# Optimization experiments

Hardware: AMD Instinct MI355X
Metric: run time of the kernel (lower is better)

The kernel has to match this reference:

```python
import jax, jax.numpy as jnp
import numpy as np

NUM_NODES = 100000
OUT_CHANNELS = 64
NUM_EDGES = 3200000


def setup_inputs() -> dict:
    key = jax.random.key(0)
    k1, k2, k3 = jax.random.split(key, 3)
    edge_index = jax.random.randint(k1, (2, NUM_EDGES), 0, NUM_NODES, dtype=jnp.int64) if jax.config.jax_enable_x64 else jax.random.randint(k1, (2, NUM_EDGES), 0, NUM_NODES, dtype=jnp.int32)
    # nn.Linear default init: U(-1/sqrt(fan_in), 1/sqrt(fan_in)); use randn-scale for a correctness baseline
    W_weight = jax.random.normal(k2, (OUT_CHANNELS, NUM_NODES), dtype=jnp.float32) * (1.0 / np.sqrt(NUM_NODES))
    W_bias = jax.random.normal(k3, (OUT_CHANNELS,), dtype=jnp.float32) * (1.0 / np.sqrt(NUM_NODES))
    return {"edge_index": edge_index, "W_weight": W_weight, "W_bias": W_bias}


def reference(edge_index, W_weight, W_bias):
    # A is the [N, N] binary COO adjacency (duplicate edges sum, matching
    # an uncoalesced torch sparse COO matmul). logits = A @ W_weight.T + b.
    num_nodes = W_weight.shape[1]
    row = edge_index[0] - jnp.min(edge_index[0])  # row = row - row.min()
    col = edge_index[1]
    Wt = W_weight.T  # [N, C]
    # SpMM as gather + segment-sum: logits[i] = sum_{(i,j) in E} Wt[j]
    logits = jax.ops.segment_sum(Wt[col], row, num_segments=num_nodes)  # [N, C]
    logits = logits + W_bias
    return jax.nn.log_softmax(logits, axis=1)
```

## Files before the change

### kernel.cpp

```cpp
#include <hip/hip_runtime.h>
#include <hip/hip_bf16.h>
#include <limits.h>

#define NUM_NODES 100000
#define OUT_CH 64
#define NUM_EDGES 3200000
#define BROWS 64
#define BSHIFT 6
#define NBUCK 1563
#define NPBLK 256
#define EPB (NUM_EDGES / NPBLK)
#define I4PB (EPB / 4)
#define STAGECAP 4096
#define NTRANS 1563

__global__ __launch_bounds__(256) void LINK_62689342652831_mintrans_kernel(
    const float* __restrict__ W, unsigned short* __restrict__ Wtb,
    const int* __restrict__ rows, int* __restrict__ minp) {
    __shared__ float tile[64][65];
    if (blockIdx.x < NTRANS) {
        int n0 = blockIdx.x * 64;
        int tx = threadIdx.x & 63;
        int ty = threadIdx.x >> 6;
        for (int c = ty; c < 64; c += 4) {
            int n = n0 + tx;
            tile[c][tx] = (n < NUM_NODES) ? W[(size_t)c * NUM_NODES + n] : 0.0f;
        }
        __syncthreads();
        for (int i = ty; i < 64; i += 4) {
            int n = n0 + i;
            if (n < NUM_NODES) {
                __hip_bfloat16 bv = __float2bfloat16(tile[tx][i]);
                Wtb[(size_t)n * OUT_CH + tx] = *(unsigned short*)&bv;
            }
        }
    } else {
        int blk = blockIdx.x - NTRANS;
        int tid = blk * 256 + threadIdx.x;
        int stride = 256 * 256;
        const int4* r4 = (const int4*)rows;
        int m = INT_MAX;
        for (int i = tid; i < NUM_EDGES / 4; i += stride) {
            int4 v = r4[i];
            m = min(m, min(min(v.x, v.y), min(v.z, v.w)));
        }
        for (int off = 32; off > 0; off >>= 1) m = min(m, __shfl_xor(m, off, 64));
        int* sm = (int*)tile;
        if ((threadIdx.x & 63) == 0) sm[threadIdx.x >> 6] = m;
        __syncthreads();
        if (threadIdx.x == 0) {
            int mm = min(min(sm[0], sm[1]), min(sm[2], sm[3]));
            atomicMin(minp, mm);
        }
    }
}

__global__ __launch_bounds__(512) void LINK_62689342652831_hist2d_kernel(
    const int* __restrict__ rows, const int* __restrict__ minp,
    int* __restrict__ hist2d) {
    __shared__ int h[NBUCK];
    for (int i = threadIdx.x; i < NBUCK; i += 512) h[i] = 0;
    __syncthreads();
    int minv = *minp;
    int blk = blockIdx.x;
    const int4* r4 = (const int4*)rows;
    for (int i = threadIdx.x; i < I4PB; i += 512) {
        int4 v = r4[blk * I4PB + i];
        atomicAdd(&h[(unsigned)(v.x - minv) >> BSHIFT], 1);
        atomicAdd(&h[(unsigned)(v.y - minv) >> BSHIFT], 1);
        atomicAdd(&h[(unsigned)(v.z - minv) >> BSHIFT], 1);
        atomicAdd(&h[(unsigned)(v.w - minv) >> BSHIFT], 1);
    }
    __syncthreads();
    for (int i = threadIdx.x; i < NBUCK; i += 512) hist2d[blk * NBUCK + i] = h[i];
}

__global__ __launch_bounds__(512) void LINK_62689342652831_colscan_kernel(
    int* __restrict__ hist2d, int* __restrict__ totals) {
    int lane = threadIdx.x & 63;
    int wid = threadIdx.x >> 6;
    int b = blockIdx.x * 8 + wid;
    if (b >= NBUCK) return;
    int carry = 0;
    for (int rnd = 0; rnd < NPBLK / 64; ++rnd) {
        int blk = rnd * 64 + lane;
        int v = hist2d[blk * NBUCK + b];
        int x = v;
        for (int off = 1; off < 64; off <<= 1) {
            int y = __shfl_up(x, off, 64);
            if (lane >= off) x += y;
        }
        hist2d[blk * NBUCK + b] = x - v + carry;
        carry += __shfl(x, 63, 64);
    }
    if (lane == 0) totals[b] = carry;
}

__global__ __launch_bounds__(1024) void LINK_62689342652831_bscan_kernel(
    const int* __restrict__ totals, int* __restrict__ bstart) {
    __shared__ int ss[1024];
    int t = threadIdx.x;
    int i0 = 2 * t, i1 = 2 * t + 1;
    int v0 = (i0 < NBUCK) ? totals[i0] : 0;
    int v1 = (i1 < NBUCK) ? totals[i1] : 0;
    int p1 = v0 + v1;
    ss[t] = p1;
    __syncthreads();
    for (int off = 1; off < 1024; off <<= 1) {
        int x = (t >= off) ? ss[t - off] : 0;
        __syncthreads();
        ss[t] += x;
        __syncthreads();
    }
    int texcl = ss[t] - p1;
    if (i0 < NBUCK) bstart[i0] = texcl;
    if (i1 < NBUCK) bstart[i1] = texcl + v0;
    if (t == 1023) bstart[NBUCK] = ss[1023];
}

__global__ __launch_bounds__(512) void LINK_62689342652831_part_kernel(
    const int* __restrict__ rows, const int* __restrict__ cols,
    const int* __restrict__ minp, const int* __restrict__ hist2d,
    const int* __restrict__ bstart, unsigned int* __restrict__ packed) {
    __shared__ int offs_l[NBUCK];
    __shared__ int lcur[NBUCK];
    int blk = blockIdx.x;
    for (int i = threadIdx.x; i < NBUCK; i += 512) {
        offs_l[i] = bstart[i] + hist2d[blk * NBUCK + i];
        lcur[i] = 0;
    }
    __syncthreads();
    int minv = *minp;
    const int4* r4 = (const int4*)rows;
    const int4* c4 = (const int4*)cols;
    for (int i = threadIdx.x; i < I4PB; i += 512) {
        int4 rv = r4[blk * I4PB + i];
        int4 cv = c4[blk * I4PB + i];
#pragma unroll
        for (int k = 0; k < 4; ++k) {
            int r = ((k == 0) ? rv.x : (k == 1) ? rv.y : (k == 2) ? rv.z : rv.w) - minv;
            int c = (k == 0) ? cv.x : (k == 1) ? cv.y : (k == 2) ? cv.z : cv.w;
            int b = (unsigned)r >> BSHIFT;
            int pos = offs_l[b] + atomicAdd(&lcur[b], 1);
            packed[pos] = ((unsigned)(r & (BROWS - 1)) << 17) | (unsigned)c;
        }
    }
}

__global__ __launch_bounds__(256) void LINK_62689342652831_spmm_kernel(
    const unsigned int* __restrict__ packed, const int* __restrict__ bstart,
    const unsigned short* __restrict__ Wtb, const float* __restrict__ bias,
    float* __restrict__ out) {
    __shared__ unsigned int sorted[STAGECAP];
    __shared__ int rhist[BROWS];
    __shared__ int rstart[BROWS + 1];
    __shared__ int rcur[BROWS];

    int lane = threadIdx.x & 63;
    int wid = threadIdx.x >> 6;
    int b = blockIdx.x;
    int s = bstart[b], e = bstart[b + 1];
    int n = e - s;

    if (n <= STAGECAP) {
        if (threadIdx.x < BROWS) rhist[threadIdx.x] = 0;
        __syncthreads();
        for (int i = threadIdx.x; i < n; i += 256)
            atomicAdd(&rhist[packed[s + i] >> 17], 1);
        __syncthreads();
        if (threadIdx.x < 64) {
            int c0 = rhist[lane];
            int x0 = c0;
            for (int off = 1; off < 64; off <<= 1) {
                int y0 = __shfl_up(x0, off, 64);
                if (lane >= off) x0 += y0;
            }
            rstart[lane] = x0 - c0;
            rcur[lane] = x0 - c0;
            if (lane == 63) rstart[64] = x0;
        }
        __syncthreads();
        for (int i = threadIdx.x; i < n; i += 256) {
            unsigned int u = packed[s + i];
            int pos = atomicAdd(&rcur[u >> 17], 1);
            sorted[pos] = u;
        }
        __syncthreads();

        const uint2* Wt2 = (const uint2*)Wtb;
        int q = lane >> 4;
        int ql = lane & 15;
        float b0 = bias[4 * ql], b1 = bias[4 * ql + 1],
              b2 = bias[4 * ql + 2], b3 = bias[4 * ql + 3];

        for (int r = wid; r < BROWS; r += 4) {
            int gr = b * BROWS + r;
            if (gr >= NUM_NODES) continue;
            int s0 = rstart[r], e0 = rstart[r + 1];
            float a0 = 0, a1 = 0, a2 = 0, a3 = 0;
            int i = s0 + q;
            for (; i + 4 < e0; i += 8) {
                unsigned int ua = sorted[i], ub = sorted[i + 4];
                uint2 wa = Wt2[(size_t)(ua & 0x1FFFF) * 16 + ql];
                uint2 wb = Wt2[(size_t)(ub & 0x1FFFF) * 16 + ql];
                a0 += __uint_as_float(wa.x << 16);
                a1 += __uint_as_float(wa.x & 0xFFFF0000u);
                a2 += __uint_as_float(wa.y << 16);
                a3 += __uint_as_float(wa.y & 0xFFFF0000u);
                a0 += __uint_as_float(wb.x << 16);
                a1 += __uint_as_float(wb.x & 0xFFFF0000u);
                a2 += __uint_as_float(wb.y << 16);
                a3 += __uint_as_float(wb.y & 0xFFFF0000u);
            }
            for (; i < e0; i += 4) {
                unsigned int u = sorted[i];
                uint2 w = Wt2[(size_t)(u & 0x1FFFF) * 16 + ql];
                a0 += __uint_as_float(w.x << 16);
                a1 += __uint_as_float(w.x & 0xFFFF0000u);
                a2 += __uint_as_float(w.y << 16);
                a3 += __uint_as_float(w.y & 0xFFFF0000u);
            }
            a0 += __shfl_xor(a0, 32, 64); a1 += __shfl_xor(a1, 32, 64);
            a2 += __shfl_xor(a2, 32, 64); a3 += __shfl_xor(a3, 32, 64);
            a0 += __shfl_xor(a0, 16, 64); a1 += __shfl_xor(a1, 16, 64);
            a2 += __shfl_xor(a2, 16, 64); a3 += __shfl_xor(a3, 16, 64);

            float x0 = a0 + b0, x1 = a1 + b1, x2 = a2 + b2, x3 = a3 + b3;
            float m = fmaxf(fmaxf(x0, x1), fmaxf(x2, x3));
            for (int off = 8; off > 0; off >>= 1) m = fmaxf(m, __shfl_xor(m, off, 64));
            float ssum = expf(x0 - m) + expf(x1 - m) + expf(x2 - m) + expf(x3 - m);
            for (int off = 8; off > 0; off >>= 1) ssum += __shfl_xor(ssum, off, 64);
            float l = m + logf(ssum);
            if (lane < 16) {
                float4 o = {x0 - l, x1 - l, x2 - l, x3 - l};
                *(float4*)&out[(size_t)gr * OUT_CH + 4 * ql] = o;
            }
        }
    } else {
        float* acc = (float*)sorted;
        for (int i = threadIdx.x; i < BROWS * OUT_CH; i += 256) acc[i] = 0.0f;
        __syncthreads();
        for (int i = s + wid; i < e; i += 4) {
            unsigned int u = packed[i];
            float v = __uint_as_float((unsigned int)Wtb[(size_t)(u & 0x1FFFF) * OUT_CH + lane] << 16);
            atomicAdd(&acc[(u >> 17) * OUT_CH + lane], v);
        }
        __syncthreads();
        float bsv = bias[lane];
        for (int r = wid; r < BROWS; r += 4) {
            int gr = b * BROWS + r;
            if (gr >= NUM_NODES) continue;
            float x = acc[r * OUT_CH + lane] + bsv;
            float m = x;
            for (int off = 32; off > 0; off >>= 1) m = fmaxf(m, __shfl_xor(m, off, 64));
            float ex = expf(x - m);
            float ssum = ex;
            for (int off = 32; off > 0; off >>= 1) ssum += __shfl_xor(ssum, off, 64);
            out[(size_t)gr * OUT_CH + lane] = x - m - logf(ssum);
        }
    }
}

__global__ void LINK_62689342652831_minf_kernel(const int* __restrict__ rows, int n,
                                                int* __restrict__ minp) {
    int tid = blockIdx.x * blockDim.x + threadIdx.x;
    int stride = gridDim.x * blockDim.x;
    int m = INT_MAX;
    for (int i = tid; i < n; i += stride) m = min(m, rows[i]);
    for (int off = 32; off > 0; off >>= 1) m = min(m, __shfl_xor(m, off, 64));
    if ((threadIdx.x & 63) == 0) atomicMin(minp, m);
}

__global__ void LINK_62689342652831_scatter_kernel(const int* __restrict__ rows,
                                                   const int* __restrict__ cols,
                                                   const float* __restrict__ W,
                                                   const int* __restrict__ minp,
                                                   float* __restrict__ out) {
    int lane = threadIdx.x & 63;
    int gw = (blockIdx.x * blockDim.x + threadIdx.x) >> 6;
    int nw = (gridDim.x * blockDim.x) >> 6;
    int minv = *minp;
    for (int e = gw; e < NUM_EDGES; e += nw) {
        int r = rows[e] - minv;
        int c = cols[e];
        float v = W[(size_t)lane * NUM_NODES + c];
        unsafeAtomicAdd(&out[(size_t)r * 64 + lane], v);
    }
}

__global__ void LINK_62689342652831_logsoftmax_kernel(float* __restrict__ out,
                                                      const float* __restrict__ bias) {
    int lane = threadIdx.x & 63;
    int gw = (blockIdx.x * blockDim.x + threadIdx.x) >> 6;
    int nw = (gridDim.x * blockDim.x) >> 6;
    float b = bias[lane];
    for (int r = gw; r < NUM_NODES; r += nw) {
        float x = out[(size_t)r * 64 + lane] + b;
        float m = x;
        for (int off = 32; off > 0; off >>= 1) m = fmaxf(m, __shfl_xor(m, off, 64));
        float e = expf(x - m);
        float s = e;
        for (int off = 32; off > 0; off >>= 1) s += __shfl_xor(s, off, 64);
        out[(size_t)r * 64 + lane] = x - m - logf(s);
    }
}

extern "C" void kernel_launch(void* const* d_in, const int* in_sizes, int n_in,
                              void* d_out, int out_size, void* d_ws, size_t ws_size,
                              hipStream_t stream) {
    const int* edges = (const int*)d_in[0];
    const int* rows = edges;
    const int* cols = edges + NUM_EDGES;
    const float* W = (const float*)d_in[1];
    const float* bias = (const float*)d_in[2];
    float* out = (float*)d_out;

    char* ws = (char*)d_ws;
    const size_t OFF_MIN = 0;
    const size_t OFF_BSTART = 256;
    const size_t OFF_TOT = 8192;
    const size_t OFF_H2D = 16384;
    const size_t OFF_PACKED = 2 * 1024 * 1024;
    const size_t OFF_WTB = OFF_PACKED + (size_t)NUM_EDGES * 4;
    const size_t need = OFF_WTB + (size_t)NUM_NODES * OUT_CH * 2;

    int* minp = (int*)(ws + OFF_MIN);
    int* bstart = (int*)(ws + OFF_BSTART);
    int* totals = (int*)(ws + OFF_TOT);
    int* hist2d = (int*)(ws + OFF_H2D);
    unsigned int* packed = (unsigned int*)(ws + OFF_PACKED);
    unsigned short* Wtb = (unsigned short*)(ws + OFF_WTB);

    hipMemsetAsync(minp, 0x7f, sizeof(int), stream);

    if (ws_size >= need) {
        LINK_62689342652831_mintrans_kernel<<<NTRANS + 256, 256, 0, stream>>>(W, Wtb, rows, minp);
        LINK_62689342652831_hist2d_kernel<<<NPBLK, 512, 0, stream>>>(rows, minp, hist2d);
        LINK_62689342652831_colscan_kernel<<<(NBUCK + 7) / 8, 512, 0, stream>>>(hist2d, totals);
        LINK_62689342652831_bscan_kernel<<<1, 1024, 0, stream>>>(totals, bstart);
        LINK_62689342652831_part_kernel<<<NPBLK, 512, 0, stream>>>(rows, cols, minp, hist2d,
                                                                   bstart, packed);
        LINK_62689342652831_spmm_kernel<<<NBUCK, 256, 0, stream>>>(packed, bstart, Wtb,
                                                                   bias, out);
    } else {
        LINK_62689342652831_minf_kernel<<<2048, 256, 0, stream>>>(rows, NUM_EDGES, minp);
        hipMemsetAsync(d_out, 0, (size_t)out_size * sizeof(float), stream);
        LINK_62689342652831_scatter_kernel<<<2048, 256, 0, stream>>>(rows, cols, W, minp, out);
        LINK_62689342652831_logsoftmax_kernel<<<4096, 256, 0, stream>>>(out, bias);
    }
}
```

Before: 136.9 us.

## Bucket by raw row and use sub-bucket global cursors for partitioning

Builds the row histogram on raw row ids inside the transpose/min kernel instead of after the min is known, accumulating into a global sub-bucketed histogram with 16 sub-slots per bucket. This drops the separate histogram and column-scan kernels. The partition kernel now claims slots with global atomics on the sub-bucket cursors instead of shared per-block offsets. The min offset is applied only in the SpMM kernel, which launches extra blocks to cover shifted buckets. This cuts kernel launches and passes over the rows, at the cost of global atomic contention in partitioning and a larger single-block scan. Edge order within a bucket becomes nondeterministic, and raw row ids at or above 100032 would overflow the bucket arrays.

```diff
diff --git a/kernel.cpp b/kernel.cpp
--- a/kernel.cpp
+++ b/kernel.cpp
@@ -8,15 +8,18 @@
 #define BROWS 64
 #define BSHIFT 6
 #define NBUCK 1563
+#define NBUCK_EXT 3125
+#define NSUB 16
+#define NSS (NBUCK * NSUB)
 #define NPBLK 256
 #define EPB (NUM_EDGES / NPBLK)
 #define I4PB (EPB / 4)
 #define STAGECAP 4096
 #define NTRANS 1563
 
-__global__ __launch_bounds__(256) void LINK_62689342652831_mintrans_kernel(
+__global__ __launch_bounds__(256) void LINK_62689342652831_mth_kernel(
     const float* __restrict__ W, unsigned short* __restrict__ Wtb,
-    const int* __restrict__ rows, int* __restrict__ minp) {
+    const int* __restrict__ rows, int* __restrict__ minp, int* __restrict__ ghist) {
     __shared__ float tile[64][65];
     if (blockIdx.x < NTRANS) {
         int n0 = blockIdx.x * 64;
@@ -36,75 +39,46 @@
         }
     } else {
         int blk = blockIdx.x - NTRANS;
-        int tid = blk * 256 + threadIdx.x;
-        int stride = 256 * 256;
+        int sub = blk & (NSUB - 1);
+        int* h = (int*)tile;
+        int* sm = (int*)tile + 4096;
+        for (int i = threadIdx.x; i < NBUCK; i += 256) h[i] = 0;
+        __syncthreads();
         const int4* r4 = (const int4*)rows;
         int m = INT_MAX;
-        for (int i = tid; i < NUM_EDGES / 4; i += stride) {
-            int4 v = r4[i];
+        for (int i = threadIdx.x; i < I4PB; i += 256) {
+            int4 v = r4[blk * I4PB + i];
             m = min(m, min(min(v.x, v.y), min(v.z, v.w)));
+            atomicAdd(&h[(unsigned)v.x >> BSHIFT], 1);
+            atomicAdd(&h[(unsigned)v.y >> BSHIFT], 1);
+            atomicAdd(&h[(unsigned)v.z >> BSHIFT], 1);
+            atomicAdd(&h[(unsigned)v.w >> BSHIFT], 1);
         }
         for (int off = 32; off > 0; off >>= 1) m = min(m, __shfl_xor(m, off, 64));
-        int* sm = (int*)tile;
         if ((threadIdx.x & 63) == 0) sm[threadIdx.x >> 6] = m;
         __syncthreads();
-        if (threadIdx.x == 0) {
-            int mm = min(min(sm[0], sm[1]), min(sm[2], sm[3]));
-            atomicMin(minp, mm);
-        }
-    }
-}
-
-__global__ __launch_bounds__(512) void LINK_62689342652831_hist2d_kernel(
-    const int* __restrict__ rows, const int* __restrict__ minp,
-    int* __restrict__ hist2d) {
-    __shared__ int h[NBUCK];
-    for (int i = threadIdx.x; i < NBUCK; i += 512) h[i] = 0;
-    __syncthreads();
-    int minv = *minp;
-    int blk = blockIdx.x;
-    const int4* r4 = (const int4*)rows;
-    for (int i = threadIdx.x; i < I4PB; i += 512) {
-        int4 v = r4[blk * I4PB + i];
-        atomicAdd(&h[(unsigned)(v.x - minv) >> BSHIFT], 1);
-        atomicAdd(&h[(unsigned)(v.y - minv) >> BSHIFT], 1);
-        atomicAdd(&h[(unsigned)(v.z - minv) >> BSHIFT], 1);
-        atomicAdd(&h[(unsigned)(v.w - minv) >> BSHIFT], 1);
-    }
-    __syncthreads();
-    for (int i = threadIdx.x; i < NBUCK; i += 512) hist2d[blk * NBUCK + i] = h[i];
-}
-
-__global__ __launch_bounds__(512) void LINK_62689342652831_colscan_kernel(
-    int* __restrict__ hist2d, int* __restrict__ totals) {
-    int lane = threadIdx.x & 63;
-    int wid = threadIdx.x >> 6;
-    int b = blockIdx.x * 8 + wid;
-    if (b >= NBUCK) return;
-    int carry = 0;
-    for (int rnd = 0; rnd < NPBLK / 64; ++rnd) {
-        int blk = rnd * 64 + lane;
-        int v = hist2d[blk * NBUCK + b];
-        int x = v;
-        for (int off = 1; off < 64; off <<= 1) {
-            int y = __shfl_up(x, off, 64);
-            if (lane >= off) x += y;
-        }
-        hist2d[blk * NBUCK + b] = x - v + carry;
-        carry += __shfl(x, 63, 64);
-    }
-    if (lane == 0) totals[b] = carry;
+        for (int i = threadIdx.x; i < NBUCK; i += 256)
+            if (h[i]) atomicAdd(&ghist[i * NSUB + sub], h[i]);
+        if (threadIdx.x == 0)
+            atomicMin(minp, min(min(sm[0], sm[1]), min(sm[2], sm[3])));
+    }
 }
 
 __global__ __launch_bounds__(1024) void LINK_62689342652831_bscan_kernel(
-    const int* __restrict__ totals, int* __restrict__ bstart) {
+    const int* __restrict__ ghist, int* __restrict__ sstart, int* __restrict__ cursor) {
     __shared__ int ss[1024];
+    const int PT = 25;
     int t = threadIdx.x;
-    int i0 = 2 * t, i1 = 2 * t + 1;
-    int v0 = (i0 < NBUCK) ? totals[i0] : 0;
-    int v1 = (i1 < NBUCK) ? totals[i1] : 0;
-    int p1 = v0 + v1;
-    ss[t] = p1;
+    int base = t * PT;
+    int v[PT];
+    int run = 0;
+#pragma unroll
+    for (int k = 0; k < PT; ++k) {
+        int idx = base + k;
+        v[k] = (idx < NSS) ? ghist[idx] : 0;
+        run += v[k];
+    }
+    ss[t] = run;
     __syncthreads();
     for (int off = 1; off < 1024; off <<= 1) {
         int x = (t >= off) ? ss[t - off] : 0;
@@ -112,25 +86,21 @@
         ss[t] += x;
         __syncthreads();
     }
-    int texcl = ss[t] - p1;
-    if (i0 < NBUCK) bstart[i0] = texcl;
-    if (i1 < NBUCK) bstart[i1] = texcl + v0;
-    if (t == 1023) bstart[NBUCK] = ss[1023];
+    int acc = ss[t] - run;
+#pragma unroll
+    for (int k = 0; k < PT; ++k) {
+        int idx = base + k;
+        if (idx < NSS) { sstart[idx] = acc; cursor[idx] = acc; }
+        acc += v[k];
+    }
+    if (t == 1023) sstart[NSS] = acc;
 }
 
 __global__ __launch_bounds__(512) void LINK_62689342652831_part_kernel(
     const int* __restrict__ rows, const int* __restrict__ cols,
-    const int* __restrict__ minp, const int* __restrict__ hist2d,
-    const int* __restrict__ bstart, unsigned int* __restrict__ packed) {
-    __shared__ int offs_l[NBUCK];
-    __shared__ int lcur[NBUCK];
+    int* __restrict__ cursor, unsigned int* __restrict__ packed) {
     int blk = blockIdx.x;
-    for (int i = threadIdx.x; i < NBUCK; i += 512) {
-        offs_l[i] = bstart[i] + hist2d[blk * NBUCK + i];
-        lcur[i] = 0;
-    }
-    __syncthreads();
-    int minv = *minp;
+    int sub = blk & (NSUB - 1);
     const int4* r4 = (const int4*)rows;
     const int4* c4 = (const int4*)cols;
     for (int i = threadIdx.x; i < I4PB; i += 512) {
@@ -138,19 +108,19 @@
         int4 cv = c4[blk * I4PB + i];
 #pragma unroll
         for (int k = 0; k < 4; ++k) {
-            int r = ((k == 0) ? rv.x : (k == 1) ? rv.y : (k == 2) ? rv.z : rv.w) - minv;
+            int r = (k == 0) ? rv.x : (k == 1) ? rv.y : (k == 2) ? rv.z : rv.w;
             int c = (k == 0) ? cv.x : (k == 1) ? cv.y : (k == 2) ? cv.z : cv.w;
             int b = (unsigned)r >> BSHIFT;
-            int pos = offs_l[b] + atomicAdd(&lcur[b], 1);
+            int pos = atomicAdd(&cursor[b * NSUB + sub], 1);
             packed[pos] = ((unsigned)(r & (BROWS - 1)) << 17) | (unsigned)c;
         }
     }
 }
 
 __global__ __launch_bounds__(256) void LINK_62689342652831_spmm_kernel(
-    const unsigned int* __restrict__ packed, const int* __restrict__ bstart,
+    const unsigned int* __restrict__ packed, const int* __restrict__ sstart,
     const unsigned short* __restrict__ Wtb, const float* __restrict__ bias,
-    float* __restrict__ out) {
+    const int* __restrict__ minp, float* __restrict__ out) {
     __shared__ unsigned int sorted[STAGECAP];
     __shared__ int rhist[BROWS];
     __shared__ int rstart[BROWS + 1];
@@ -159,7 +129,10 @@
     int lane = threadIdx.x & 63;
     int wid = threadIdx.x >> 6;
     int b = blockIdx.x;
-    int s = bstart[b], e = bstart[b + 1];
+    int minv = *minp;
+    if (b * BROWS - minv >= NUM_NODES) return;
+    int s = 0, e = 0;
+    if (b < NBUCK) { s = sstart[b * NSUB]; e = sstart[(b + 1) * NSUB]; }
     int n = e - s;
 
     if (n <= STAGECAP) {
@@ -194,8 +167,8 @@
               b2 = bias[4 * ql + 2], b3 = bias[4 * ql + 3];
 
         for (int r = wid; r < BROWS; r += 4) {
-            int gr = b * BROWS + r;
-            if (gr >= NUM_NODES) continue;
+            int gr = b * BROWS + r - minv;
+            if (gr < 0 || gr >= NUM_NODES) continue;
             int s0 = rstart[r], e0 = rstart[r + 1];
             float a0 = 0, a1 = 0, a2 = 0, a3 = 0;
             int i = s0 + q;
@@ -248,8 +221,8 @@
         __syncthreads();
         float bsv = bias[lane];
         for (int r = wid; r < BROWS; r += 4) {
-            int gr = b * BROWS + r;
-            if (gr >= NUM_NODES) continue;
+            int gr = b * BROWS + r - minv;
+            if (gr < 0 || gr >= NUM_NODES) continue;
             float x = acc[r * OUT_CH + lane] + bsv;
             float m = x;
             for (int off = 32; off > 0; off >>= 1) m = fmaxf(m, __shfl_xor(m, off, 64));
@@ -317,31 +290,30 @@
 
     char* ws = (char*)d_ws;
     const size_t OFF_MIN = 0;
-    const size_t OFF_BSTART = 256;
-    const size_t OFF_TOT = 8192;
-    const size_t OFF_H2D = 16384;
-    const size_t OFF_PACKED = 2 * 1024 * 1024;
+    const size_t OFF_GHIST = 1024;
+    const size_t OFF_SSTART = 256 * 1024;
+    const size_t OFF_CUR = 512 * 1024;
+    const size_t OFF_PACKED = 1024 * 1024;
     const size_t OFF_WTB = OFF_PACKED + (size_t)NUM_EDGES * 4;
     const size_t need = OFF_WTB + (size_t)NUM_NODES * OUT_CH * 2;
 
     int* minp = (int*)(ws + OFF_MIN);
-    int* bstart = (int*)(ws + OFF_BSTART);
-    int* totals = (int*)(ws + OFF_TOT);
-    int* hist2d = (int*)(ws + OFF_H2D);
+    int* ghist = (int*)(ws + OFF_GHIST);
+    int* sstart = (int*)(ws + OFF_SSTART);
+    int* cursor = (int*)(ws + OFF_CUR);
     unsigned int* packed = (unsigned int*)(ws + OFF_PACKED);
     unsigned short* Wtb = (unsigned short*)(ws + OFF_WTB);
 
     hipMemsetAsync(minp, 0x7f, sizeof(int), stream);
 
     if (ws_size >= need) {
-        LINK_62689342652831_mintrans_kernel<<<NTRANS + 256, 256, 0, stream>>>(W, Wtb, rows, minp);
-        LINK_62689342652831_hist2d_kernel<<<NPBLK, 512, 0, stream>>>(rows, minp, hist2d);
-        LINK_62689342652831_colscan_kernel<<<(NBUCK + 7) / 8, 512, 0, stream>>>(hist2d, totals);
-        LINK_62689342652831_bscan_kernel<<<1, 1024, 0, stream>>>(totals, bstart);
-        LINK_62689342652831_part_kernel<<<NPBLK, 512, 0, stream>>>(rows, cols, minp, hist2d,
-                                                                   bstart, packed);
-        LINK_62689342652831_spmm_kernel<<<NBUCK, 256, 0, stream>>>(packed, bstart, Wtb,
-                                                                   bias, out);
+        hipMemsetAsync(ghist, 0, (size_t)NSS * sizeof(int), stream);
+        LINK_62689342652831_mth_kernel<<<NTRANS + NPBLK, 256, 0, stream>>>(W, Wtb, rows,
+                                                                           minp, ghist);
+        LINK_62689342652831_bscan_kernel<<<1, 1024, 0, stream>>>(ghist, sstart, cursor);
+        LINK_62689342652831_part_kernel<<<NPBLK, 512, 0, stream>>>(rows, cols, cursor, packed);
+        LINK_62689342652831_spmm_kernel<<<NBUCK_EXT, 256, 0, stream>>>(packed, sstart, Wtb,
+                                                                       bias, minp, out);
     } else {
         LINK_62689342652831_minf_kernel<<<2048, 256, 0, stream>>>(rows, NUM_EDGES, minp);
         hipMemsetAsync(d_out, 0, (size_t)out_size * sizeof(float), stream);
```

Measured after the change: 296.9 us. 2.17x slower.

## Store transposed weights in scaled FP8 and fuse row histogram into min/transpose pass

Applied to the files above, without the earlier changes.

Quantizes the transposed weight table to scaled FP8 E4M3 instead of bf16, which halves the bytes gathered per edge in the SpMM. It also merges the histogram pass into the min-reduction/transpose kernel by bucketing on raw row ids, and applies the row-min offset later in the SpMM, launching extra blocks to cover the shift. This removes one kernel launch and one full read of the rows array. The cost is a large loss of precision from FP8, which may break tolerance, plus some idle extra SpMM blocks.

```diff
diff --git a/kernel.cpp b/kernel.cpp
--- a/kernel.cpp
+++ b/kernel.cpp
@@ -1,5 +1,6 @@
 #include <hip/hip_runtime.h>
 #include <hip/hip_bf16.h>
+#include <hip/hip_fp8.h>
 #include <limits.h>
 
 #define NUM_NODES 100000
@@ -8,15 +9,26 @@
 #define BROWS 64
 #define BSHIFT 6
 #define NBUCK 1563
+#define NBUCK_EXT 3125
 #define NPBLK 256
 #define EPB (NUM_EDGES / NPBLK)
 #define I4PB (EPB / 4)
 #define STAGECAP 4096
 #define NTRANS 1563
-
-__global__ __launch_bounds__(256) void LINK_62689342652831_mintrans_kernel(
-    const float* __restrict__ W, unsigned short* __restrict__ Wtb,
-    const int* __restrict__ rows, int* __restrict__ minp) {
+#define FP8_SCALE 256.0f
+#define FP8_INV (1.0f / 256.0f)
+
+typedef float v2f __attribute__((ext_vector_type(2)));
+
+__device__ __forceinline__ float fp8_decode_slow(unsigned b) {
+    unsigned s = b >> 7, e = (b >> 3) & 0xF, m = b & 7;
+    float v = (e == 0) ? ldexpf((float)m, -9) : ldexpf((float)(8 + m), (int)e - 10);
+    return s ? -v : v;
+}
+
+__global__ __launch_bounds__(256) void LINK_62689342652831_mth_kernel(
+    const float* __restrict__ W, unsigned char* __restrict__ Wt8,
+    const int* __restrict__ rows, int* __restrict__ minp, int* __restrict__ hist2d) {
     __shared__ float tile[64][65];
     if (blockIdx.x < NTRANS) {
         int n0 = blockIdx.x * 64;
@@ -30,49 +42,33 @@
         for (int i = ty; i < 64; i += 4) {
             int n = n0 + i;
             if (n < NUM_NODES) {
-                __hip_bfloat16 bv = __float2bfloat16(tile[tx][i]);
-                Wtb[(size_t)n * OUT_CH + tx] = *(unsigned short*)&bv;
+                __hip_fp8_e4m3 q(FP8_SCALE * tile[tx][i]);
+                Wt8[(size_t)n * OUT_CH + tx] = *reinterpret_cast<unsigned char*>(&q);
             }
         }
     } else {
         int blk = blockIdx.x - NTRANS;
-        int tid = blk * 256 + threadIdx.x;
-        int stride = 256 * 256;
+        int* h = (int*)tile;
+        int* sm = (int*)tile + 2048;
+        for (int i = threadIdx.x; i < NBUCK; i += 256) h[i] = 0;
+        __syncthreads();
         const int4* r4 = (const int4*)rows;
         int m = INT_MAX;
-        for (int i = tid; i < NUM_EDGES / 4; i += stride) {
-            int4 v = r4[i];
+        for (int i = threadIdx.x; i < I4PB; i += 256) {
+            int4 v = r4[blk * I4PB + i];
             m = min(m, min(min(v.x, v.y), min(v.z, v.w)));
+            atomicAdd(&h[(unsigned)v.x >> BSHIFT], 1);
+            atomicAdd(&h[(unsigned)v.y >> BSHIFT], 1);
+            atomicAdd(&h[(unsigned)v.z >> BSHIFT], 1);
+            atomicAdd(&h[(unsigned)v.w >> BSHIFT], 1);
         }
         for (int off = 32; off > 0; off >>= 1) m = min(m, __shfl_xor(m, off, 64));
-        int* sm = (int*)tile;
         if ((threadIdx.x & 63) == 0) sm[threadIdx.x >> 6] = m;
         __syncthreads();
-        if (threadIdx.x == 0) {
-            int mm = min(min(sm[0], sm[1]), min(sm[2], sm[3]));
-            atomicMin(minp, mm);
-        }
-    }
-}
-
-__global__ __launch_bounds__(512) void LINK_62689342652831_hist2d_kernel(
-    const int* __restrict__ rows, const int* __restrict__ minp,
-    int* __restrict__ hist2d) {
-    __shared__ int h[NBUCK];
-    for (int i = threadIdx.x; i < NBUCK; i += 512) h[i] = 0;
-    __syncthreads();
-    int minv = *minp;
-    int blk = blockIdx.x;
-    const int4* r4 = (const int4*)rows;
-    for (int i = threadIdx.x; i < I4PB; i += 512) {
-        int4 v = r4[blk * I4PB + i];
-        atomicAdd(&h[(unsigned)(v.x - minv) >> BSHIFT], 1);
-        atomicAdd(&h[(unsigned)(v.y - minv) >> BSHIFT], 1);
-        atomicAdd(&h[(unsigned)(v.z - minv) >> BSHIFT], 1);
-        atomicAdd(&h[(unsigned)(v.w - minv) >> BSHIFT], 1);
-    }
-    __syncthreads();
-    for (int i = threadIdx.x; i < NBUCK; i += 512) hist2d[blk * NBUCK + i] = h[i];
+        for (int i = threadIdx.x; i < NBUCK; i += 256) hist2d[blk * NBUCK + i] = h[i];
+        if (threadIdx.x == 0)
+            atomicMin(minp, min(min(sm[0], sm[1]), min(sm[2], sm[3])));
+    }
 }
 
 __global__ __launch_bounds__(512) void LINK_62689342652831_colscan_kernel(
@@ -120,8 +116,8 @@
 
 __global__ __launch_bounds__(512) void LINK_62689342652831_part_kernel(
     const int* __restrict__ rows, const int* __restrict__ cols,
-    const int* __restrict__ minp, const int* __restrict__ hist2d,
-    const int* __restrict__ bstart, unsigned int* __restrict__ packed) {
+    const int* __restrict__ hist2d, const int* __restrict__ bstart,
+    unsigned int* __restrict__ packed) {
     __shared__ int offs_l[NBUCK];
     __shared__ int lcur[NBUCK];
     int blk = blockIdx.x;
@@ -130,7 +126,6 @@
         lcur[i] = 0;
     }
     __syncthreads();
-    int minv = *minp;
     const int4* r4 = (const int4*)rows;
     const int4* c4 = (const int4*)cols;
     for (int i = threadIdx.x; i < I4PB; i += 512) {
@@ -138,7 +133,7 @@
         int4 cv = c4[blk * I4PB + i];
 #pragma unroll
         for (int k = 0; k < 4; ++k) {
-            int r = ((k == 0) ? rv.x : (k == 1) ? rv.y : (k == 2) ? rv.z : rv.w) - minv;
+            int r = (k == 0) ? rv.x : (k == 1) ? rv.y : (k == 2) ? rv.z : rv.w;
             int c = (k == 0) ? cv.x : (k == 1) ? cv.y : (k == 2) ? cv.z : cv.w;
             int b = (unsigned)r >> BSHIFT;
             int pos = offs_l[b] + atomicAdd(&lcur[b], 1);
@@ -149,8 +144,8 @@
 
 __global__ __launch_bounds__(256) void LINK_62689342652831_spmm_kernel(
     const unsigned int* __restrict__ packed, const int* __restrict__ bstart,
-    const unsigned short* __restrict__ Wtb, const float* __restrict__ bias,
-    float* __restrict__ out) {
+    const unsigned char* __restrict__ Wt8, const float* __restrict__ bias,
+    const int* __restrict__ minp, float* __restrict__ out) {
     __shared__ unsigned int sorted[STAGECAP];
     __shared__ int rhist[BROWS];
     __shared__ int rstart[BROWS + 1];
@@ -159,7 +154,10 @@
     int lane = threadIdx.x & 63;
     int wid = threadIdx.x >> 6;
     int b = blockIdx.x;
-    int s = bstart[b], e = bstart[b + 1];
+    int minv = *minp;
+    if (b * BROWS - minv >= NUM_NODES) return;
+    int s = 0, e = 0;
+    if (b < NBUCK) { s = bstart[b]; e = bstart[b + 1]; }
     int n = e - s;
 
     if (n <= STAGECAP) {
@@ -187,45 +185,56 @@
         }
         __syncthreads();
 
-        const uint2* Wt2 = (const uint2*)Wtb;
+        const unsigned int* Wt1 = (const unsigned int*)Wt8;
         int q = lane >> 4;
         int ql = lane & 15;
         float b0 = bias[4 * ql], b1 = bias[4 * ql + 1],
               b2 = bias[4 * ql + 2], b3 = bias[4 * ql + 3];
 
         for (int r = wid; r < BROWS; r += 4) {
-            int gr = b * BROWS + r;
-            if (gr >= NUM_NODES) continue;
+            int gr = b * BROWS + r - minv;
+            if (gr < 0 || gr >= NUM_NODES) continue;
             int s0 = rstart[r], e0 = rstart[r + 1];
             float a0 = 0, a1 = 0, a2 = 0, a3 = 0;
             int i = s0 + q;
             for (; i + 4 < e0; i += 8) {
                 unsigned int ua = sorted[i], ub = sorted[i + 4];
-                uint2 wa = Wt2[(size_t)(ua & 0x1FFFF) * 16 + ql];
-                uint2 wb = Wt2[(size_t)(ub & 0x1FFFF) * 16 + ql];
-                a0 += __uint_as_float(wa.x << 16);
-                a1 += __uint_as_float(wa.x & 0xFFFF0000u);
-                a2 += __uint_as_float(wa.y << 16);
-                a3 += __uint_as_float(wa.y & 0xFFFF0000u);
-                a0 += __uint_as_float(wb.x << 16);
-                a1 += __uint_as_float(wb.x & 0xFFFF0000u);
-                a2 += __uint_as_float(wb.y << 16);
-                a3 += __uint_as_float(wb.y & 0xFFFF0000u);
+                unsigned int wa = Wt1[(size_t)(ua & 0x1FFFF) * 16 + ql];
+                unsigned int wb = Wt1[(size_t)(ub & 0x1FFFF) * 16 + ql];
+#if __has_builtin(__builtin_amdgcn_cvt_pk_f32_fp8)
+                v2f la = __builtin_amdgcn_cvt_pk_f32_fp8((int)wa, false);
+                v2f ha = __builtin_amdgcn_cvt_pk_f32_fp8((int)wa, true);
+                v2f lb = __builtin_amdgcn_cvt_pk_f32_fp8((int)wb, false);
+                v2f hb = __builtin_amdgcn_cvt_pk_f32_fp8((int)wb, true);
+                a0 += la.x + lb.x; a1 += la.y + lb.y;
+                a2 += ha.x + hb.x; a3 += ha.y + hb.y;
+#else
+                a0 += fp8_decode_slow(wa & 0xFF) + fp8_decode_slow(wb & 0xFF);
+                a1 += fp8_decode_slow((wa >> 8) & 0xFF) + fp8_decode_slow((wb >> 8) & 0xFF);
+                a2 += fp8_decode_slow((wa >> 16) & 0xFF) + fp8_decode_slow((wb >> 16) & 0xFF);
+                a3 += fp8_decode_slow(wa >> 24) + fp8_decode_slow(wb >> 24);
+#endif
             }
             for (; i < e0; i += 4) {
-                unsigned int u = sorted[i];
-                uint2 w = Wt2[(size_t)(u & 0x1FFFF) * 16 + ql];
-                a0 += __uint_as_float(w.x << 16);
-                a1 += __uint_as_float(w.x & 0xFFFF0000u);
-                a2 += __uint_as_float(w.y << 16);
-                a3 += __uint_as_float(w.y & 0xFFFF0000u);
+                unsigned int w = Wt1[(size_t)(sorted[i] & 0x1FFFF) * 16 + ql];
+#if __has_builtin(__builtin_amdgcn_cvt_pk_f32_fp8)
+                v2f lo = __builtin_amdgcn_cvt_pk_f32_fp8((int)w, false);
+                v2f hi = __builtin_amdgcn_cvt_pk_f32_fp8((int)w, true);
+                a0 += lo.x; a1 += lo.y; a2 += hi.x; a3 += hi.y;
+#else
+                a0 += fp8_decode_slow(w & 0xFF);
+                a1 += fp8_decode_slow((w >> 8) & 0xFF);
+                a2 += fp8_decode_slow((w >> 16) & 0xFF);
+                a3 += fp8_decode_slow(w >> 24);
+#endif
             }
             a0 += __shfl_xor(a0, 32, 64); a1 += __shfl_xor(a1, 32, 64);
             a2 += __shfl_xor(a2, 32, 64); a3 += __shfl_xor(a3, 32, 64);
             a0 += __shfl_xor(a0, 16, 64); a1 += __shfl_xor(a1, 16, 64);
             a2 += __shfl_xor(a2, 16, 64); a3 += __shfl_xor(a3, 16, 64);
 
-            float x0 = a0 + b0, x1 = a1 + b1, x2 = a2 + b2, x3 = a3 + b3;
+            float x0 = a0 * FP8_INV + b0, x1 = a1 * FP8_INV + b1;
+            float x2 = a2 * FP8_INV + b2, x3 = a3 * FP8_INV + b3;
             float m = fmaxf(fmaxf(x0, x1), fmaxf(x2, x3));
             for (int off = 8; off > 0; off >>= 1) m = fmaxf(m, __shfl_xor(m, off, 64));
             float ssum = expf(x0 - m) + expf(x1 - m) + expf(x2 - m) + expf(x3 - m);
@@ -242,15 +251,15 @@
         __syncthreads();
         for (int i = s + wid; i < e; i += 4) {
             unsigned int u = packed[i];
-            float v = __uint_as_float((unsigned int)Wtb[(size_t)(u & 0x1FFFF) * OUT_CH + lane] << 16);
+            float v = fp8_decode_slow(Wt8[(size_t)(u & 0x1FFFF) * OUT_CH + lane]);
             atomicAdd(&acc[(u >> 17) * OUT_CH + lane], v);
         }
         __syncthreads();
         float bsv = bias[lane];
         for (int r = wid; r < BROWS; r += 4) {
-            int gr = b * BROWS + r;
-            if (gr >= NUM_NODES) continue;
-            float x = acc[r * OUT_CH + lane] + bsv;
+            int gr = b * BROWS + r - minv;
+            if (gr < 0 || gr >= NUM_NODES) continue;
+            float x = acc[r * OUT_CH + lane] * FP8_INV + bsv;
             float m = x;
             for (int off = 32; off > 0; off >>= 1) m = fmaxf(m, __shfl_xor(m, off, 64));
             float ex = expf(x - m);
@@ -317,31 +326,31 @@
 
     char* ws = (char*)d_ws;
     const size_t OFF_MIN = 0;
-    const size_t OFF_BSTART = 256;
-    const size_t OFF_TOT = 8192;
-    const size_t OFF_H2D = 16384;
+    const size_t OFF_TOT = 1024;
+    const size_t OFF_BSTART = 16384;
+    const size_t OFF_H2D = 32768;
     const size_t OFF_PACKED = 2 * 1024 * 1024;
-    const size_t OFF_WTB = OFF_PACKED + (size_t)NUM_EDGES * 4;
-    const size_t need = OFF_WTB + (size_t)NUM_NODES * OUT_CH * 2;
+    const size_t OFF_WT8 = OFF_PACKED + (size_t)NUM_EDGES * 4;
+    const size_t need = OFF_WT8 + (size_t)NUM_NODES * OUT_CH;
 
     int* minp = (int*)(ws + OFF_MIN);
+    int* totals = (int*)(ws + OFF_TOT);
     int* bstart = (int*)(ws + OFF_BSTART);
-    int* totals = (int*)(ws + OFF_TOT);
     int* hist2d = (int*)(ws + OFF_H2D);
     unsigned int* packed = (unsigned int*)(ws + OFF_PACKED);
-    unsigned short* Wtb = (unsigned short*)(ws + OFF_WTB);
+    unsigned char* Wt8 = (unsigned char*)(ws + OFF_WT8);
 
     hipMemsetAsync(minp, 0x7f, sizeof(int), stream);
 
     if (ws_size >= need) {
-        LINK_62689342652831_mintrans_kernel<<<NTRANS + 256, 256, 0, stream>>>(W, Wtb, rows, minp);
-        LINK_62689342652831_hist2d_kernel<<<NPBLK, 512, 0, stream>>>(rows, minp, hist2d);
+        LINK_62689342652831_mth_kernel<<<NTRANS + NPBLK, 256, 0, stream>>>(W, Wt8, rows,
+                                                                           minp, hist2d);
         LINK_62689342652831_colscan_kernel<<<(NBUCK + 7) / 8, 512, 0, stream>>>(hist2d, totals);
         LINK_62689342652831_bscan_kernel<<<1, 1024, 0, stream>>>(totals, bstart);
-        LINK_62689342652831_part_kernel<<<NPBLK, 512, 0, stream>>>(rows, cols, minp, hist2d,
+        LINK_62689342652831_part_kernel<<<NPBLK, 512, 0, stream>>>(rows, cols, hist2d,
                                                                    bstart, packed);
-        LINK_62689342652831_spmm_kernel<<<NBUCK, 256, 0, stream>>>(packed, bstart, Wtb,
-                                                                   bias, out);
+        LINK_62689342652831_spmm_kernel<<<NBUCK_EXT, 256, 0, stream>>>(packed, bstart, Wt8,
+                                                                       bias, minp, out);
     } else {
         LINK_62689342652831_minf_kernel<<<2048, 256, 0, stream>>>(rows, NUM_EDGES, minp);
         hipMemsetAsync(d_out, 0, (size_t)out_size * sizeof(float), stream);
```

Result: faster. 127.4 us (-7.0%).
